# Performance work log

Hardware: AMD Instinct MI355X
Metric: run time of the kernel (lower is better)

## Reference

```python
import jax, jax.numpy as jnp
import numpy as np

C, H, W = 64, 282, 282
PILLAR_SIZE = 0.16
RANGE_MIN = -22.0


def _scatter_forward(PFN_input, PFN_output):
    # PFN_input: [B, 2, P, 1] pillar (x, y) coords; PFN_output: [B, C, P] features
    x = PFN_input[:, 0, :, 0]  # [B, P]
    y = PFN_input[:, 1, :, 0]  # [B, P]
    valid = x != 0  # original uses nonzero(PFN_input[b,0,:,0]) as pillar list
    # digitize into grid cells (equivalent of get_grid over arange(-22,22,0.16))
    xg = jnp.floor((x - RANGE_MIN) / PILLAR_SIZE).astype(jnp.int32)
    yg = jnp.floor((y - RANGE_MIN) / PILLAR_SIZE).astype(jnp.int32)
    # route invalid pillars to an out-of-bounds index; jax scatter drops OOB updates
    xg = jnp.where(valid, jnp.clip(xg, 0, W - 1), W)
    yg = jnp.where(valid, jnp.clip(yg, 0, H - 1), H)

    def scatter_one(xgb, ygb, feats):  # xgb,ygb: [P]; feats: [C, P]
        canvas = jnp.zeros((C, H, W), feats.dtype)
        return canvas.at[:, ygb, xgb].set(feats)

    return jax.vmap(scatter_one)(xg, yg, PFN_output)  # [B, C, H, W]


def setup_inputs() -> dict:
    key = jax.random.key(0)
    k1, k2 = jax.random.split(key)
    B, P = 4, 12000
    PFN_input = jax.random.uniform(k1, (B, 2, P, 1), dtype=jnp.float32,
                                   minval=-22.0, maxval=22.0)
    PFN_output = jax.random.normal(k2, (B, C, P), dtype=jnp.float32)
    return {"PFN_input": PFN_input, "PFN_output": PFN_output}


def reference(PFN_input, PFN_output):
    return _scatter_forward(PFN_input, PFN_output)
```

## Files before the change

### kernel.cpp

```cpp
#include <hip/hip_runtime.h>

#define NB 4
#define NC 64
#define NH 282
#define NW 282
#define NP 12000
#define HWC (NH * NW)
#define QHW (HWC / 4)
#define CLAIM_INTS (NB * HWC)

__device__ __align__(16) int g_claim[CLAIM_INTS];

__global__ void pps_init_kernel() {
    int gid = blockIdx.x * blockDim.x + threadIdx.x;
    if (gid < CLAIM_INTS / 4) {
        ((int4*)g_claim)[gid] = make_int4(-1, -1, -1, -1);
    }
}

__global__ void pps_claim_kernel(const float* __restrict__ pfn_in) {
    int gid = blockIdx.x * blockDim.x + threadIdx.x;
    if (gid >= NB * NP) return;
    int b = gid / NP;
    int p = gid - b * NP;
    const float* base = pfn_in + (size_t)b * 2 * NP;
    float x = base[p];
    if (x == 0.0f) return;
    float y = base[NP + p];
    float tx = (x + 22.0f) * 6.25f;
    float ty = (y + 22.0f) * 6.25f;
    int xg = (int)floorf(tx);
    int yg = (int)floorf(ty);
    xg = min(max(xg, 0), NW - 1);
    yg = min(max(yg, 0), NH - 1);
    atomicMax(&g_claim[b * HWC + yg * NW + xg], p);
}

__global__ void pps_fill_kernel(const float* __restrict__ pfn_out,
                                float4* __restrict__ out) {
    int gid = blockIdx.x * blockDim.x + threadIdx.x;
    if (gid >= NB * NC * QHW) return;
    int plane = gid / QHW;
    int q = gid - plane * QHW;
    int b = plane >> 6;
    const int4 cl = ((const int4*)(g_claim + (size_t)b * HWC))[q];
    const float* row = pfn_out + (size_t)plane * NP;
    float4 v;
    v.x = (cl.x >= 0) ? row[cl.x] : 0.0f;
    v.y = (cl.y >= 0) ? row[cl.y] : 0.0f;
    v.z = (cl.z >= 0) ? row[cl.z] : 0.0f;
    v.w = (cl.w >= 0) ? row[cl.w] : 0.0f;
    out[gid] = v;
}

extern "C" void kernel_launch(void* const* d_in, const int* in_sizes, int n_in,
                              void* d_out, int out_size, void* d_ws, size_t ws_size,
                              hipStream_t stream) {
    const float* pfn_in  = (const float*)d_in[0];
    const float* pfn_out = (const float*)d_in[1];
    float* out = (float*)d_out;
    (void)d_ws; (void)ws_size;

    {
        int total = CLAIM_INTS / 4;
        int threads = 256;
        pps_init_kernel<<<(total + threads - 1) / threads, threads, 0, stream>>>();
    }
    {
        int total = NB * NP;
        int threads = 256;
        pps_claim_kernel<<<(total + threads - 1) / threads, threads, 0, stream>>>(pfn_in);
    }
    {
        int total = NB * NC * QHW;
        int threads = 256;
        pps_fill_kernel<<<(total + threads - 1) / threads, threads, 0, stream>>>(pfn_out, (float4*)out);
    }
}
```

Before: 118.9 us.

## Stage feature row in LDS and gather from shared memory in fill kernel

The fill kernel now assigns each workgroup a slice of one (batch, channel) plane. It first copies that plane's 12000-float feature row into shared memory, then gathers claimed pillar values from LDS instead of from global memory. This replaces scattered global loads with one coalesced row load per block, at the cost of reloading the row SPLIT times per plane and using 48KB of LDS per block, which may limit occupancy.

```diff
diff --git a/kernel.cpp b/kernel.cpp
--- a/kernel.cpp
+++ b/kernel.cpp
@@ -8,6 +8,7 @@
 #define HWC (NH * NW)
 #define QHW (HWC / 4)
 #define CLAIM_INTS (NB * HWC)
+#define SPLIT 8
 
 __device__ __align__(16) int g_claim[CLAIM_INTS];
 
@@ -27,30 +28,41 @@
     float x = base[p];
     if (x == 0.0f) return;
     float y = base[NP + p];
-    float tx = (x + 22.0f) * 6.25f;
-    float ty = (y + 22.0f) * 6.25f;
-    int xg = (int)floorf(tx);
-    int yg = (int)floorf(ty);
+    int xg = (int)floorf((x + 22.0f) * 6.25f);
+    int yg = (int)floorf((y + 22.0f) * 6.25f);
     xg = min(max(xg, 0), NW - 1);
     yg = min(max(yg, 0), NH - 1);
     atomicMax(&g_claim[b * HWC + yg * NW + xg], p);
 }
 
-__global__ void pps_fill_kernel(const float* __restrict__ pfn_out,
-                                float4* __restrict__ out) {
-    int gid = blockIdx.x * blockDim.x + threadIdx.x;
-    if (gid >= NB * NC * QHW) return;
-    int plane = gid / QHW;
-    int q = gid - plane * QHW;
+__global__ __launch_bounds__(256) void pps_fill2_kernel(
+        const float* __restrict__ pfn_out, float4* __restrict__ out) {
+    __shared__ float row[NP];
+    int wg = blockIdx.x;
+    int s = wg & (SPLIT - 1);
+    int plane = wg / SPLIT;
     int b = plane >> 6;
-    const int4 cl = ((const int4*)(g_claim + (size_t)b * HWC))[q];
-    const float* row = pfn_out + (size_t)plane * NP;
-    float4 v;
-    v.x = (cl.x >= 0) ? row[cl.x] : 0.0f;
-    v.y = (cl.y >= 0) ? row[cl.y] : 0.0f;
-    v.z = (cl.z >= 0) ? row[cl.z] : 0.0f;
-    v.w = (cl.w >= 0) ? row[cl.w] : 0.0f;
-    out[gid] = v;
+
+    const float4* src4 = (const float4*)(pfn_out + (size_t)plane * NP);
+    for (int i = threadIdx.x; i < NP / 4; i += 256) {
+        ((float4*)row)[i] = src4[i];
+    }
+    __syncthreads();
+
+    const int4* cl = (const int4*)(g_claim + (size_t)b * HWC);
+    float4* dst = out + (size_t)plane * QHW;
+    const int chunk = (QHW + SPLIT - 1) / SPLIT;
+    int q0 = s * chunk;
+    int q1 = min(q0 + chunk, QHW);
+    for (int q = q0 + (int)threadIdx.x; q < q1; q += 256) {
+        int4 c4 = cl[q];
+        float4 v;
+        v.x = (c4.x >= 0) ? row[c4.x] : 0.0f;
+        v.y = (c4.y >= 0) ? row[c4.y] : 0.0f;
+        v.z = (c4.z >= 0) ? row[c4.z] : 0.0f;
+        v.w = (c4.w >= 0) ? row[c4.w] : 0.0f;
+        dst[q] = v;
+    }
 }
 
 extern "C" void kernel_launch(void* const* d_in, const int* in_sizes, int n_in,
@@ -72,8 +84,7 @@
         pps_claim_kernel<<<(total + threads - 1) / threads, threads, 0, stream>>>(pfn_in);
     }
     {
-        int total = NB * NC * QHW;
-        int threads = 256;
-        pps_fill_kernel<<<(total + threads - 1) / threads, threads, 0, stream>>>(pfn_out, (float4*)out);
+        int blocks = NB * NC * SPLIT;
+        pps_fill2_kernel<<<blocks, 256, 0, stream>>>(pfn_out, (float4*)out);
     }
 }
```

Result: slower. 126.6 us (+6.5%).
